# Kernel tuning notes

Hardware: AMD Instinct MI355X
Metric: run time of the kernel (lower is better)

## Reference

```python
import jax, jax.numpy as jnp
import numpy as np

D, H, W = 128, 128, 128
MAX_R = 2  # static; equals min(ceil(max radius_vox), 20) given scales <= 0.01 -> radius <= 1.92
N_PTS = 100000


def quaternion_to_rotation_matrix(q):
    # q: (N, 4) as (w, x, y, z)
    q = q / jnp.linalg.norm(q, axis=-1, keepdims=True)
    w, x, y, z = q[..., 0], q[..., 1], q[..., 2], q[..., 3]
    r00 = 1 - 2 * (y * y + z * z); r01 = 2 * (x * y - w * z); r02 = 2 * (x * z + w * y)
    r10 = 2 * (x * y + w * z); r11 = 1 - 2 * (x * x + z * z); r12 = 2 * (y * z - w * x)
    r20 = 2 * (x * z - w * y); r21 = 2 * (y * z + w * x); r22 = 1 - 2 * (x * x + y * y)
    return jnp.stack([r00, r01, r02, r10, r11, r12, r20, r21, r22], axis=-1).reshape(q.shape[0], 3, 3)


def setup_inputs() -> dict:
    key = jax.random.key(0)
    k1, k2, k3, k4 = jax.random.split(key, 4)
    positions = jax.random.uniform(k1, (N_PTS, 3), minval=-1.0, maxval=1.0, dtype=jnp.float32)
    scales = jax.random.uniform(k2, (N_PTS, 3), minval=0.002, maxval=0.01, dtype=jnp.float32)
    rotations = jax.random.normal(k3, (N_PTS, 4), dtype=jnp.float32)
    density = jax.random.normal(k4, (N_PTS,), dtype=jnp.float32)
    return {"positions": positions, "scales": scales, "rotations": rotations,
            "density": density, "chunk_size": 4096}


def reference(positions, scales, rotations, density, chunk_size):
    # chunk_size only affects torch memory staging, not the math (single logical chunk here)
    shape_t = jnp.array([D, H, W], dtype=jnp.float32)
    center = (positions + 1.0) * 0.5 * shape_t - 0.5            # (N,3) voxel-space centers
    Rm = quaternion_to_rotation_matrix(rotations)                # (N,3,3)
    S_inv = 1.0 / (scales + 1e-8)                                # (N,3)
    L = Rm * S_inv[:, None, :]                                   # scale columns, as in torch R * S_inv.unsqueeze(1)
    cov_inv = jnp.einsum('nij,nkj->nik', L, L)                   # L @ L^T, (N,3,3)

    k_rng = jnp.arange(-MAX_R, MAX_R + 1)
    kz, ky, kx = jnp.meshgrid(k_rng, k_rng, k_rng, indexing='ij')
    offsets = jnp.stack([kz, ky, kx], axis=-1).reshape(-1, 3).astype(jnp.float32)  # (K,3), K=(2r+1)^3

    gc = jnp.round(center)[:, None, :] + offsets[None, :, :]     # (N,K,3) global voxel coords
    gz, gy, gx = gc[..., 0], gc[..., 1], gc[..., 2]
    valid = (gz >= 0) & (gz < D) & (gy >= 0) & (gy < H) & (gx >= 0) & (gx < W)

    diff_norm = (gc - center[:, None, :]) / (shape_t * 0.5)      # (N,K,3)
    mahal = jnp.einsum('nkd,nde,nke->nk', diff_norm, cov_inv, diff_norm)  # (N,K)
    mask = valid & (mahal <= 9.0)

    vals = jnp.where(mask, jnp.exp(-0.5 * mahal), 0.0) * density[:, None]  # (N,K)
    flat_idx = (gz.astype(jnp.int32) * (H * W) + gy.astype(jnp.int32) * W + gx.astype(jnp.int32))
    flat_idx = jnp.where(mask, flat_idx, 0)                      # masked entries carry zero value

    volume = jnp.zeros(D * H * W, dtype=jnp.float32).at[flat_idx.reshape(-1)].add(vals.reshape(-1))
    return volume.reshape(D, H, W)
```

## Files before the change

### kernel.cpp

```cpp
#include <hip/hip_runtime.h>


#define VOX 128
#define T0 4
#define T1 8
#define T2 32
#define NT0 (VOX / T0)
#define NT1 (VOX / T1)
#define NT2 (VOX / T2)
#define NCELL (NT0 * NT1 * NT2)
#define CAP 256
#define CAPQ 1280


__global__ __launch_bounds__(256) void bin_points(
    const float* __restrict__ positions,
    const float* __restrict__ scales,
    const float* __restrict__ rotations,
    const float* __restrict__ density,
    unsigned int* __restrict__ counts,
    unsigned int* __restrict__ bins,
    float4* __restrict__ rec,
    int n)
{
    const int i = blockIdx.x * blockDim.x + threadIdx.x;
    if (i >= n) return;

    const float c0 = (positions[3 * i + 0] + 1.0f) * 64.0f - 0.5f;
    const float c1 = (positions[3 * i + 1] + 1.0f) * 64.0f - 0.5f;
    const float c2 = (positions[3 * i + 2] + 1.0f) * 64.0f - 0.5f;

    float qw = rotations[4 * i + 0];
    float qx = rotations[4 * i + 1];
    float qy = rotations[4 * i + 2];
    float qz = rotations[4 * i + 3];
    const float qn = rsqrtf(qw * qw + qx * qx + qy * qy + qz * qz);
    qw *= qn; qx *= qn; qy *= qn; qz *= qn;

    const float r00 = 1.0f - 2.0f * (qy * qy + qz * qz);
    const float r01 = 2.0f * (qx * qy - qw * qz);
    const float r02 = 2.0f * (qx * qz + qw * qy);
    const float r10 = 2.0f * (qx * qy + qw * qz);
    const float r11 = 1.0f - 2.0f * (qx * qx + qz * qz);
    const float r12 = 2.0f * (qy * qz - qw * qx);
    const float r20 = 2.0f * (qx * qz - qw * qy);
    const float r21 = 2.0f * (qy * qz + qw * qx);
    const float r22 = 1.0f - 2.0f * (qx * qx + qy * qy);

    const float si0 = 1.0f / (scales[3 * i + 0] + 1e-8f);
    const float si1 = 1.0f / (scales[3 * i + 1] + 1e-8f);
    const float si2 = 1.0f / (scales[3 * i + 2] + 1e-8f);

    rec[4 * i + 0] = make_float4(c0, c1, c2, density[i]);
    rec[4 * i + 1] = make_float4(si0 * r00, si0 * r10, si0 * r20, 0.0f);
    rec[4 * i + 2] = make_float4(si1 * r01, si1 * r11, si1 * r21, 0.0f);
    rec[4 * i + 3] = make_float4(si2 * r02, si2 * r12, si2 * r22, 0.0f);

    const int b0 = (int)rintf(c0);
    const int b1 = (int)rintf(c1);
    const int b2 = (int)rintf(c2);

    const int cell = ((b0 / T0) * NT1 + (b1 / T1)) * NT2 + (b2 / T2);
    const unsigned entry = (unsigned)i |
                           ((unsigned)(b0 & (T0 - 1)) << 17) |
                           ((unsigned)(b1 & (T1 - 1)) << 19) |
                           ((unsigned)(b2 & (T2 - 1)) << 22);
    const unsigned slot = atomicAdd(&counts[cell], 1u);
    if (slot < CAP) bins[cell * CAP + slot] = entry;
}

__global__ __launch_bounds__(256) void splat_tiles(
    const unsigned int* __restrict__ counts,
    const unsigned int* __restrict__ bins,
    const float4* __restrict__ rec,
    float* __restrict__ volume)
{
    __shared__ float tile[T0 * T1 * T2];
    __shared__ int seg_cell[27];
    __shared__ int seg_base[27];
    __shared__ int seg_start[28];
    __shared__ unsigned queue[CAPQ];
    __shared__ int qcount;

    const int t = threadIdx.x;
    const int tx = blockIdx.x, ty = blockIdx.y, tz = blockIdx.z;
    const int X0 = tz * T0, X1 = ty * T1, X2 = tx * T2;

    for (int v = t; v < T0 * T1 * T2; v += 256) tile[v] = 0.0f;
    if (t == 0) qcount = 0;

    const int z0 = max(tz - 1, 0), z1 = min(tz + 1, NT0 - 1);
    const int y0 = max(ty - 1, 0), y1 = min(ty + 1, NT1 - 1);
    const int x0 = max(tx - 1, 0), x1 = min(tx + 1, NT2 - 1);
    const int nz = z1 - z0 + 1, ny = y1 - y0 + 1, nx = x1 - x0 + 1;
    const int ncells = nz * ny * nx;

    if (t < ncells) {
        const int kz = t / (ny * nx);
        const int r  = t - kz * (ny * nx);
        const int ky = r / nx;
        const int kx = r - ky * nx;
        const int cz = z0 + kz, cy = y0 + ky, cx = x0 + kx;
        const int cell = (cz * NT1 + cy) * NT2 + cx;
        seg_cell[t] = cell;
        seg_base[t] = (cz * T0 << 16) | (cy * T1 << 8) | (cx * T2);
        int c = (int)counts[cell];
        seg_start[t] = (c > CAP) ? CAP : c;
    }
    __syncthreads();
    if (t == 0) {
        int acc = 0;
        for (int k = 0; k < ncells; ++k) {
            const int c = seg_start[k];
            seg_start[k] = acc;
            acc += c;
        }
        seg_start[ncells] = acc;
    }
    __syncthreads();

    const int total = seg_start[ncells];
    int s = 0;
    for (int j = t; j < total; j += 256) {
        while (j >= seg_start[s + 1]) ++s;
        const unsigned e = bins[seg_cell[s] * CAP + (j - seg_start[s])];
        const int sb = seg_base[s];
        const int b0 = ((sb >> 16) & 255) + ((e >> 17) & (T0 - 1));
        const int b1 = ((sb >> 8) & 255) + ((e >> 19) & (T1 - 1));
        const int b2 = (sb & 255) + ((e >> 22) & (T2 - 1));

        const int lo0 = max(b0 - 2, X0), hi0 = min(b0 + 2, X0 + T0 - 1);
        const bool hit1 = (b1 >= X1 - 2) & (b1 <= X1 + T1 + 1);
        const bool hit2 = (b2 >= X2 - 2) & (b2 <= X2 + T2 + 1);
        if (lo0 > hi0 || !hit1 || !hit2) continue;

        const unsigned p = e & 0x1FFFFu;
        const unsigned rel1 = (unsigned)(b1 - (X1 - 2));
        const unsigned rel2 = (unsigned)(b2 - (X2 - 2));
        for (int g0 = lo0; g0 <= hi0; ++g0) {
            const unsigned item = p | ((unsigned)(g0 - X0) << 17) |
                                  (rel1 << 19) | (rel2 << 23);
            const int slot = atomicAdd(&qcount, 1);
            if (slot < CAPQ) queue[slot] = item;
        }
    }
    __syncthreads();

    int nq = qcount; if (nq > CAPQ) nq = CAPQ;
    const float inv_half = 1.0f / 64.0f;
    for (int j = t; j < nq; j += 256) {
        const unsigned item = queue[j];
        const int p  = (int)(item & 0x1FFFFu);
        const int g0 = X0 + (int)((item >> 17) & 3u);
        const int b1 = X1 - 2 + (int)((item >> 19) & 15u);
        const int b2 = X2 - 2 + (int)((item >> 23) & 63u);

        const float4 r0 = rec[4 * p + 0];
        const float4 r1 = rec[4 * p + 1];
        const float4 r2 = rec[4 * p + 2];
        const float4 r3 = rec[4 * p + 3];

        const int lo1 = max(b1 - 2, X1), hi1 = min(b1 + 2, X1 + T1 - 1);
        const int lo2 = max(b2 - 2, X2), hi2 = min(b2 + 2, X2 + T2 - 1);

        const float d0 = ((float)g0 - r0.x) * inv_half;
        const float f0 = r1.x * d0;
        const float f1 = r2.x * d0;
        const float f2 = r3.x * d0;
        const int base0 = (g0 - X0) * T1;

        for (int g1 = lo1; g1 <= hi1; ++g1) {
            const float d1 = ((float)g1 - r0.y) * inv_half;
            const float e0 = f0 + r1.y * d1;
            const float e1 = f1 + r2.y * d1;
            const float e2 = f2 + r3.y * d1;
            const int base1 = (base0 + (g1 - X1)) * T2;
            for (int g2 = lo2; g2 <= hi2; ++g2) {
                const float d2 = ((float)g2 - r0.z) * inv_half;
                const float m0 = e0 + r1.z * d2;
                const float m1 = e1 + r2.z * d2;
                const float m2 = e2 + r3.z * d2;
                const float mah = m0 * m0 + m1 * m1 + m2 * m2;
                if (mah <= 9.0f) {
                    atomicAdd(&tile[base1 + (g2 - X2)],
                              __expf(-0.5f * mah) * r0.w);
                }
            }
        }
    }
    __syncthreads();

    const float4* tl4 = (const float4*)tile;
    const int row = t >> 3;
    const int ch  = t & 7;
    const int l0 = row >> 3;
    const int l1 = row & 7;
    const int g = ((X0 + l0) * VOX + (X1 + l1)) * VOX + X2 + ch * 4;
    ((float4*)volume)[g >> 2] = tl4[t];
}

extern "C" void kernel_launch(void* const* d_in, const int* in_sizes, int n_in,
                              void* d_out, int out_size, void* d_ws, size_t ws_size,
                              hipStream_t stream) {
    const float* positions = (const float*)d_in[0];
    const float* scales    = (const float*)d_in[1];
    const float* rotations = (const float*)d_in[2];
    const float* density   = (const float*)d_in[3];
    float* volume = (float*)d_out;

    const int n = in_sizes[0] / 3;

    unsigned int* counts = (unsigned int*)d_ws;
    unsigned int* bins   = (unsigned int*)((char*)d_ws + (64 << 10));
    float4* rec          = (float4*)((char*)d_ws + (4 << 20));

    hipMemsetAsync(counts, 0, NCELL * sizeof(unsigned int), stream);

    bin_points<<<(n + 255) / 256, 256, 0, stream>>>(
        positions, scales, rotations, density, counts, bins, rec, n);

    dim3 grid(NT2, NT1, NT0);
    splat_tiles<<<grid, 256, 0, stream>>>(counts, bins, rec, volume);
}
```

Measured before the change: 103.5 us.

## Precompute symmetric covariance, shrink tiles, replace shared atomics with wave prefix-sum queues

Each point now stores the six unique entries of the inverse covariance instead of the scaled rotation columns. This cuts per-point records from four float4 to three, and the inner Mahalanobis evaluation becomes an incremental quadratic form. The x tile width halves to 16 with 128-thread blocks, which doubles the grid and halves the bin capacity. Per-element shared atomic queue appends are replaced by per-wave shuffle prefix sums writing into two wave-private queues, and the cell-count scan becomes a shuffle scan. Risks are bin overflow at CAP 128 dropping points and a changed floating-point ordering.

After: 100.4 us. -3.0%, faster.

```diff
diff --git a/kernel.cpp b/kernel.cpp
--- a/kernel.cpp
+++ b/kernel.cpp
@@ -4,13 +4,13 @@
 #define VOX 128
 #define T0 4
 #define T1 8
-#define T2 32
+#define T2 16
 #define NT0 (VOX / T0)
 #define NT1 (VOX / T1)
 #define NT2 (VOX / T2)
 #define NCELL (NT0 * NT1 * NT2)
-#define CAP 256
-#define CAPQ 1280
+#define CAP 128
+#define WQ 512
 
 
 __global__ __launch_bounds__(256) void bin_points(
@@ -50,11 +50,18 @@
     const float si0 = 1.0f / (scales[3 * i + 0] + 1e-8f);
     const float si1 = 1.0f / (scales[3 * i + 1] + 1e-8f);
     const float si2 = 1.0f / (scales[3 * i + 2] + 1e-8f);
-
-    rec[4 * i + 0] = make_float4(c0, c1, c2, density[i]);
-    rec[4 * i + 1] = make_float4(si0 * r00, si0 * r10, si0 * r20, 0.0f);
-    rec[4 * i + 2] = make_float4(si1 * r01, si1 * r11, si1 * r21, 0.0f);
-    rec[4 * i + 3] = make_float4(si2 * r02, si2 * r12, si2 * r22, 0.0f);
+    const float w0 = si0 * si0, w1 = si1 * si1, w2 = si2 * si2;
+
+    const float A00 = w0 * r00 * r00 + w1 * r01 * r01 + w2 * r02 * r02;
+    const float A11 = w0 * r10 * r10 + w1 * r11 * r11 + w2 * r12 * r12;
+    const float A22 = w0 * r20 * r20 + w1 * r21 * r21 + w2 * r22 * r22;
+    const float A01 = w0 * r00 * r10 + w1 * r01 * r11 + w2 * r02 * r12;
+    const float A02 = w0 * r00 * r20 + w1 * r01 * r21 + w2 * r02 * r22;
+    const float A12 = w0 * r10 * r20 + w1 * r11 * r21 + w2 * r12 * r22;
+
+    rec[3 * i + 0] = make_float4(c0, c1, c2, density[i]);
+    rec[3 * i + 1] = make_float4(A00, A11, A22, A01);
+    rec[3 * i + 2] = make_float4(A02, A12, 0.0f, 0.0f);
 
     const int b0 = (int)rintf(c0);
     const int b1 = (int)rintf(c1);
@@ -69,7 +76,7 @@
     if (slot < CAP) bins[cell * CAP + slot] = entry;
 }
 
-__global__ __launch_bounds__(256) void splat_tiles(
+__global__ __launch_bounds__(128) void splat_tiles(
     const unsigned int* __restrict__ counts,
     const unsigned int* __restrict__ bins,
     const float4* __restrict__ rec,
@@ -79,15 +86,16 @@
     __shared__ int seg_cell[27];
     __shared__ int seg_base[27];
     __shared__ int seg_start[28];
-    __shared__ unsigned queue[CAPQ];
-    __shared__ int qcount;
+    __shared__ unsigned queue[2 * WQ];
+    __shared__ int qcount[2];
 
     const int t = threadIdx.x;
+    const int lane = t & 63;
+    const int wv = t >> 6;
     const int tx = blockIdx.x, ty = blockIdx.y, tz = blockIdx.z;
     const int X0 = tz * T0, X1 = ty * T1, X2 = tx * T2;
 
-    for (int v = t; v < T0 * T1 * T2; v += 256) tile[v] = 0.0f;
-    if (t == 0) qcount = 0;
+    for (int v = t; v < T0 * T1 * T2; v += 128) tile[v] = 0.0f;
 
     const int z0 = max(tz - 1, 0), z1 = min(tz + 1, NT0 - 1);
     const int y0 = max(ty - 1, 0), y1 = min(ty + 1, NT1 - 1);
@@ -108,79 +116,96 @@
         seg_start[t] = (c > CAP) ? CAP : c;
     }
     __syncthreads();
-    if (t == 0) {
-        int acc = 0;
-        for (int k = 0; k < ncells; ++k) {
-            const int c = seg_start[k];
-            seg_start[k] = acc;
-            acc += c;
-        }
-        seg_start[ncells] = acc;
+
+    if (t < 64) {
+        int v = (t < ncells) ? seg_start[t] : 0;
+        int inc = v;
+#pragma unroll
+        for (int off = 1; off < 32; off <<= 1) {
+            const int u = __shfl_up(inc, off, 64);
+            if (lane >= off) inc += u;
+        }
+        if (t < ncells) seg_start[t + 1] = inc;
+        if (t == 0) seg_start[0] = 0;
     }
     __syncthreads();
 
     const int total = seg_start[ncells];
     int s = 0;
-    for (int j = t; j < total; j += 256) {
-        while (j >= seg_start[s + 1]) ++s;
-        const unsigned e = bins[seg_cell[s] * CAP + (j - seg_start[s])];
-        const int sb = seg_base[s];
-        const int b0 = ((sb >> 16) & 255) + ((e >> 17) & (T0 - 1));
-        const int b1 = ((sb >> 8) & 255) + ((e >> 19) & (T1 - 1));
-        const int b2 = (sb & 255) + ((e >> 22) & (T2 - 1));
-
-        const int lo0 = max(b0 - 2, X0), hi0 = min(b0 + 2, X0 + T0 - 1);
-        const bool hit1 = (b1 >= X1 - 2) & (b1 <= X1 + T1 + 1);
-        const bool hit2 = (b2 >= X2 - 2) & (b2 <= X2 + T2 + 1);
-        if (lo0 > hi0 || !hit1 || !hit2) continue;
-
-        const unsigned p = e & 0x1FFFFu;
-        const unsigned rel1 = (unsigned)(b1 - (X1 - 2));
-        const unsigned rel2 = (unsigned)(b2 - (X2 - 2));
-        for (int g0 = lo0; g0 <= hi0; ++g0) {
-            const unsigned item = p | ((unsigned)(g0 - X0) << 17) |
-                                  (rel1 << 19) | (rel2 << 23);
-            const int slot = atomicAdd(&qcount, 1);
-            if (slot < CAPQ) queue[slot] = item;
-        }
-    }
-    __syncthreads();
-
-    int nq = qcount; if (nq > CAPQ) nq = CAPQ;
+    int wbase = 0;
+    for (int jb = wv * 64; jb < total; jb += 128) {
+        const int j = jb + lane;
+        const bool active = j < total;
+        int np = 0;
+        unsigned base_item = 0;
+        if (active) {
+            while (j >= seg_start[s + 1]) ++s;
+            const unsigned e = bins[seg_cell[s] * CAP + (j - seg_start[s])];
+            const int sb = seg_base[s];
+            const int b0 = ((sb >> 16) & 255) + ((e >> 17) & (T0 - 1));
+            const int b1 = ((sb >> 8) & 255) + ((e >> 19) & (T1 - 1));
+            const int b2 = (sb & 255) + ((e >> 22) & (T2 - 1));
+            const int lo0 = max(b0 - 2, X0), hi0 = min(b0 + 2, X0 + T0 - 1);
+            const bool hit = (lo0 <= hi0) &
+                             (b1 >= X1 - 2) & (b1 <= X1 + T1 + 1) &
+                             (b2 >= X2 - 2) & (b2 <= X2 + T2 + 1);
+            if (hit) {
+                np = hi0 - lo0 + 1;
+                base_item = (e & 0x1FFFFu) |
+                            ((unsigned)(lo0 - X0) << 17) |
+                            ((unsigned)(b1 - (X1 - 2)) << 19) |
+                            ((unsigned)(b2 - (X2 - 2)) << 23);
+            }
+        }
+        int inc = np;
+#pragma unroll
+        for (int off = 1; off < 64; off <<= 1) {
+            const int u = __shfl_up(inc, off, 64);
+            if (lane >= off) inc += u;
+        }
+        const int excl = inc - np;
+        const int tot = __shfl(inc, 63, 64);
+        for (int k = 0; k < np; ++k) {
+            const int slot = wbase + excl + k;
+            if (slot < WQ)
+                queue[wv * WQ + slot] = base_item + ((unsigned)k << 17);
+        }
+        wbase += tot;
+    }
+    if (lane == 0) qcount[wv] = (wbase > WQ) ? WQ : wbase;
+    __syncthreads();
+
+    const int q0 = qcount[0];
+    const int nq = q0 + qcount[1];
     const float inv_half = 1.0f / 64.0f;
-    for (int j = t; j < nq; j += 256) {
-        const unsigned item = queue[j];
+    for (int j = t; j < nq; j += 128) {
+        const unsigned item = (j < q0) ? queue[j] : queue[WQ + (j - q0)];
         const int p  = (int)(item & 0x1FFFFu);
         const int g0 = X0 + (int)((item >> 17) & 3u);
         const int b1 = X1 - 2 + (int)((item >> 19) & 15u);
-        const int b2 = X2 - 2 + (int)((item >> 23) & 63u);
-
-        const float4 r0 = rec[4 * p + 0];
-        const float4 r1 = rec[4 * p + 1];
-        const float4 r2 = rec[4 * p + 2];
-        const float4 r3 = rec[4 * p + 3];
+        const int b2 = X2 - 2 + (int)((item >> 23) & 31u);
+
+        const float4 r0 = rec[3 * p + 0];
+        const float4 r1 = rec[3 * p + 1];
+        const float4 r2 = rec[3 * p + 2];
 
         const int lo1 = max(b1 - 2, X1), hi1 = min(b1 + 2, X1 + T1 - 1);
         const int lo2 = max(b2 - 2, X2), hi2 = min(b2 + 2, X2 + T2 - 1);
 
         const float d0 = ((float)g0 - r0.x) * inv_half;
-        const float f0 = r1.x * d0;
-        const float f1 = r2.x * d0;
-        const float f2 = r3.x * d0;
+        const float K0 = r1.x * d0 * d0;
+        const float u1 = 2.0f * r1.w * d0;
+        const float u2 = 2.0f * r2.x * d0;
         const int base0 = (g0 - X0) * T1;
 
         for (int g1 = lo1; g1 <= hi1; ++g1) {
             const float d1 = ((float)g1 - r0.y) * inv_half;
-            const float e0 = f0 + r1.y * d1;
-            const float e1 = f1 + r2.y * d1;
-            const float e2 = f2 + r3.y * d1;
+            const float K1 = K0 + d1 * (r1.y * d1 + u1);
+            const float u3 = u2 + 2.0f * r2.y * d1;
             const int base1 = (base0 + (g1 - X1)) * T2;
             for (int g2 = lo2; g2 <= hi2; ++g2) {
                 const float d2 = ((float)g2 - r0.z) * inv_half;
-                const float m0 = e0 + r1.z * d2;
-                const float m1 = e1 + r2.z * d2;
-                const float m2 = e2 + r3.z * d2;
-                const float mah = m0 * m0 + m1 * m1 + m2 * m2;
+                const float mah = K1 + d2 * (r1.z * d2 + u3);
                 if (mah <= 9.0f) {
                     atomicAdd(&tile[base1 + (g2 - X2)],
                               __expf(-0.5f * mah) * r0.w);
@@ -191,8 +216,8 @@
     __syncthreads();
 
     const float4* tl4 = (const float4*)tile;
-    const int row = t >> 3;
-    const int ch  = t & 7;
+    const int row = t >> 2;
+    const int ch  = t & 3;
     const int l0 = row >> 3;
     const int l1 = row & 7;
     const int g = ((X0 + l0) * VOX + (X1 + l1)) * VOX + X2 + ch * 4;
@@ -220,5 +245,5 @@
         positions, scales, rotations, density, counts, bins, rec, n);
 
     dim3 grid(NT2, NT1, NT0);
-    splat_tiles<<<grid, 256, 0, stream>>>(counts, bins, rec, volume);
+    splat_tiles<<<grid, 128, 0, stream>>>(counts, bins, rec, volume);
 }
```
